# Kernel optimization log

Measured on AMD Instinct MI355X. Metric: run time of the kernel, lower is better.

## Reference

```python
import jax, jax.numpy as jnp
import numpy as np
from math import pi, sqrt, factorial

NUM_SPHERICAL = 7
NUM_RADIAL = 6
CUTOFF = 5.0


def _sph_jn_np(x, n):
    # spherical Bessel j_n(x) in float64 numpy via upward recurrence
    x = np.asarray(x, dtype=np.float64)
    jm = np.sin(x) / x
    if n == 0:
        return jm
    jc = np.sin(x) / x**2 - np.cos(x) / x
    for l in range(2, n + 1):
        jm, jc = jc, (2 * l - 1) / x * jc - jm
    return jc


def _jn_zeros(n, k):
    # first k positive zeros of j_l for l = 0..n-1 (zeros of j_l interleave those of j_{l-1})
    nz = k + n
    z = np.zeros((n, nz))
    z[0] = np.arange(1, nz + 1) * np.pi
    for l in range(1, n):
        for j in range(nz - l):
            a, b = z[l - 1, j], z[l - 1, j + 1]
            fa = _sph_jn_np(a, l)
            for _ in range(100):
                m = 0.5 * (a + b)
                fm = _sph_jn_np(m, l)
                if fa * fm <= 0:
                    b = m
                else:
                    a, fa = m, fm
            z[l, j] = 0.5 * (a + b)
    return z[:, :k]


_ZEROS_NP = _jn_zeros(NUM_SPHERICAL, NUM_RADIAL)  # (n, k)
_NORM_NP = np.array([[(0.5 * _sph_jn_np(_ZEROS_NP[l, j], l + 1) ** 2) ** -0.5
                      for j in range(NUM_RADIAL)] for l in range(NUM_SPHERICAL)])
BESSEL_ZEROS = jnp.asarray(_ZEROS_NP, dtype=jnp.float32)  # z_{l,j}
BESSEL_NORM = jnp.asarray(_NORM_NP, dtype=jnp.float32)    # sqrt(2)/|j_{l+1}(z_{l,j})|


def _rbf(dist):
    # normalized spherical Bessel basis: rbf[:, l*k + j] = norm[l,j] * j_l(z_{l,j} * dist/cutoff)
    d = dist / CUTOFF
    u = d[:, None, None] * BESSEL_ZEROS[None]  # (E, n, k)
    cols = []
    for l in range(NUM_SPHERICAL):
        x = u[:, l, :]
        jm = jnp.sin(x) / x  # j_0
        if l == 0:
            jc = jm
        else:
            jc = jnp.sin(x) / (x * x) - jnp.cos(x) / x  # j_1
        for ll in range(2, l + 1):
            jm, jc = jc, (2 * ll - 1) / x * jc - jm
        cols.append(BESSEL_NORM[l] * jc)
    return jnp.concatenate(cols, axis=1)  # (E, n*k)


def _cbf(angle, phi):
    # real spherical harmonics Y_{l,m}(angle, phi), flat order m = -l..l per l
    n = NUM_SPHERICAL
    z = jnp.cos(angle)
    s = jnp.sin(angle)
    P = {(0, 0): jnp.ones_like(z)}
    for m in range(1, n):
        P[(m, m)] = (1 - 2 * m) * s * P[(m - 1, m - 1)]  # Condon-Shortley phase included
    for m in range(0, n - 1):
        P[(m + 1, m)] = (2 * m + 1) * z * P[(m, m)]
    for m in range(n):
        for l in range(m + 2, n):
            P[(l, m)] = ((2 * l - 1) * z * P[(l - 1, m)] - (l + m - 1) * P[(l - 2, m)]) / (l - m)

    def pref(l, m):
        return sqrt((2 * l + 1) * factorial(l - m) / (4.0 * pi * factorial(l + m)))

    cols = [jnp.full_like(angle, 0.5 / sqrt(pi))]  # Y_00 constant
    for l in range(1, n):
        for m in range(-l, l + 1):
            am = abs(m)
            if m < 0:
                cols.append(sqrt(2.0) * pref(l, am) * jnp.sin(am * phi) * P[(l, am)])
            elif m == 0:
                cols.append(pref(l, 0) * P[(l, 0)])
            else:
                cols.append(sqrt(2.0) * pref(l, am) * jnp.cos(am * phi) * P[(l, am)])
    return jnp.stack(cols, axis=1)  # (T, n*n)


def setup_inputs() -> dict:
    key = jax.random.key(0)
    kd, ka, kp, ki = jax.random.split(key, 4)
    E, T = 150000, 500000
    dist = jax.random.uniform(kd, (E,), minval=0.5, maxval=5.0, dtype=jnp.float32)
    angle = jax.random.uniform(ka, (T,), minval=0.0, maxval=float(np.pi), dtype=jnp.float32)
    phi = jax.random.uniform(kp, (T,), minval=-float(np.pi), maxval=float(np.pi), dtype=jnp.float32)
    idx_kj = jax.random.randint(ki, (T,), 0, E)
    return {"dist": dist, "angle": angle, "phi": phi, "idx_kj": idx_kj}


def reference(dist, angle, phi, idx_kj):
    n, k = NUM_SPHERICAL, NUM_RADIAL
    rbf = _rbf(dist)          # (E, n*k)
    cbf = _cbf(angle, phi)    # (T, n*n)
    out = (rbf[idx_kj].reshape(-1, 1, n, k) * cbf.reshape(-1, n, n, 1)).reshape(-1, n * n * k)
    return out
```

## Files before the change

### kernel.cpp

```cpp
#include <hip/hip_runtime.h>
#include <math.h>

#ifndef M_PI
#define M_PI 3.14159265358979323846
#endif

#define NS 7
#define NK 6
#define GT 64
#define BT 256
#define NC (NS*NS)
#define NR (NS*NK)
#define NF2 147

typedef float f32x2 __attribute__((ext_vector_type(2)));
typedef float f32x4 __attribute__((ext_vector_type(4)));


__device__ void jl_pair_f(float x, int l, float& jl, float& jm1) {
  float s, c;
  __sincosf(x, &s, &c);
  float invx = 1.0f / x;
  float j0 = s * invx, jm = c * invx;
  if (l == 0) { jl = j0; jm1 = jm; return; }
  float j1 = (s * invx - c) * invx;
  for (int ll = 2; ll <= l; ++ll) {
    float t = (2.0f * ll - 1.0f) * invx * j1 - j0;
    j0 = j1; j1 = t;
  }
  jl = j1; jm1 = j0;
}

__global__ void setup_kernel(float* tab) {
  int id = threadIdx.x;
  if (id < NS * NK) {
    int l = id / NK, j = id % NK;
    float nu = l + 0.5f, mu = 4.0f * nu * nu;
    float b  = ((float)(j + 1) + 0.5f * nu - 0.25f) * (float)M_PI;
    float b8 = 8.0f * b;
    float x = b - (mu - 1.0f) / b8
                - 4.0f * (mu - 1.0f) * (7.0f * mu - 31.0f) / (3.0f * b8 * b8 * b8)
                - 32.0f * (mu - 1.0f) * (83.0f * mu * mu - 982.0f * mu + 3779.0f) /
                  (15.0f * b8 * b8 * b8 * b8 * b8);
    float jl, jm1;
    for (int it = 0; it < 5; ++it) {
      jl_pair_f(x, l, jl, jm1);
      float dj = jm1 - (l + 1.0f) / x * jl;
      x -= jl / dj;
    }
    tab[id] = x;
    jl_pair_f(x, l, jl, jm1);
    float jp1 = (2.0f * l + 1.0f) / x * jl - jm1;
    tab[NS * NK + id] = sqrtf(2.0f) / fabsf(jp1);
  }
  if (id < NC) {
    double v;
    if (id == 0) {
      v = 0.5 / sqrt(M_PI);
    } else {
      int l = 1;
      while ((l + 1) * (l + 1) <= id) ++l;
      int m  = id - l * l - l;
      int am = m < 0 ? -m : m;
      double fr = 1.0;
      for (int i2 = l - am + 1; i2 <= l + am; ++i2) fr *= (double)i2;
      double pref = sqrt((2.0 * l + 1.0) / (4.0 * M_PI * fr));
      v = (m != 0) ? sqrt(2.0) * pref : pref;
    }
    tab[2 * NS * NK + id] = (float)v;
  }
}

__global__ __launch_bounds__(BT, 6) void torsion_kernel(
    const float* __restrict__ dist, const float* __restrict__ angle,
    const float* __restrict__ phi, const int* __restrict__ idx_kj,
    const float* __restrict__ tab, float* __restrict__ out, int T) {
  __shared__ float s_cbf[GT][NC];
  __shared__ __align__(8) float s_rbf[GT][NR];
  __shared__ float s_d[GT];
  __shared__ float s_tab[133];
  __shared__ unsigned s_map2[NF2];

  const int tid = threadIdx.x;
  const int t0  = blockIdx.x * GT;
  const int nt  = min(GT, T - t0);

  float a = 0.0f, ph = 0.0f;
  if (tid < GT) {
    int t = t0 + tid;
    float dd = 1.0f;
    if (t < T) {
      dd = dist[idx_kj[t]] * 0.2f;
      a  = angle[t];
      ph = phi[t];
    }
    s_d[tid] = dd;
  }
  if (tid < 133) s_tab[tid] = tab[tid];
  if (tid < NF2) {
    auto mk = [](int cc) {
      int ii = (cc * 3121) >> 16;
      int rem2 = cc - 21 * ii;
      int jj = (rem2 * 86) >> 8;
      return (unsigned)((ii * NS + jj) | (rem2 << 8));
    };
    int cc1 = tid + 1; if (cc1 == NF2) cc1 = 0;
    s_map2[tid] = mk(tid) | (mk(cc1) << 16);
  }
  __syncthreads();

  if (tid < GT) {
    if (t0 + tid < T) {
      float z, s;
      __sincosf(a, &s, &z);
      float sp, cp;
      __sincosf(ph, &sp, &cp);
      float cmv[NS], smv[NS];
      cmv[0] = 1.0f; smv[0] = 0.0f;
      cmv[1] = cp;   smv[1] = sp;
#pragma unroll
      for (int m = 2; m < NS; ++m) {
        cmv[m] = 2.0f * cp * cmv[m - 1] - cmv[m - 2];
        smv[m] = 2.0f * cp * smv[m - 1] - smv[m - 2];
      }
      const float* coef = s_tab + 2 * NR;
      float* crow = s_cbf[tid];
      float pmm = 1.0f;
#pragma unroll
      for (int m = 0; m < NS; ++m) {
        float pl1 = pmm, pl2 = 0.0f;
#pragma unroll
        for (int l = m; l < NS; ++l) {
          float plm;
          if (l == m)          plm = pmm;
          else if (l == m + 1) plm = (float)(2 * m + 1) * z * pmm;
          else                 plm = ((float)(2 * l - 1) * z * pl1 -
                                      (float)(l + m - 1) * pl2) *
                                     (float)(1.0 / (double)(l - m));
          int cpn = l * l + l + m;
          if (m == 0) {
            crow[cpn] = coef[cpn] * plm;
          } else {
            crow[cpn] = coef[cpn] * cmv[m] * plm;
            crow[l * l + l - m] = coef[l * l + l - m] * smv[m] * plm;
          }
          pl2 = pl1; pl1 = plm;
        }
        pmm = (float)(-1 - 2 * m) * s * pmm;
      }
    }
  } else {
    int j  = tid - 64;
    int t  = j / NR;
    int cc = j - NR * t;
    int i2 = j;
    float* rlin = &s_rbf[0][0];
#pragma unroll 2
    for (int it = 0; it < 14; ++it) {
      int l = (cc * 43) >> 8;
      float x = s_d[t] * s_tab[cc];
      float sx, cx;
      __sincosf(x, &sx, &cx);
      float invx = 1.0f / x;
      float jm = sx * invx;
      float jc;
      if (l == 0) jc = jm;
      else {
        jc = (sx * invx - cx) * invx;
#pragma unroll
        for (int ll = 2; ll <= 6; ++ll) {
          if (ll <= l) {
            float tt = (float)(2 * ll - 1) * invx * jc - jm;
            jm = jc; jc = tt;
          }
        }
      }
      rlin[i2] = s_tab[NR + cc] * jc;
      i2 += 192;
      cc += 24; t += 4;
      if (cc >= NR) { cc -= NR; ++t; }
    }
  }
  __syncthreads();

  const f32x2* r2 = (const f32x2*)&s_rbf[0][0];

  if (nt == GT) {
    const int w    = tid >> 6;
    const int lane = tid & 63;
    const int n0   = w * 1176 + lane;
    int p = n0 / 147;
    int k = n0 - 147 * p;
    int cc = k << 1; if (cc >= NF2) cc -= NF2;

    f32x4* o4 = (f32x4*)out + (size_t)blockIdx.x * 4704 + n0;

    auto GATHER = [&]() -> f32x4 {
      int t2 = p << 1;
      int ta = t2 + (k >= 74 ? 1 : 0);
      int tb = t2 + (k >= 73 ? 1 : 0);
      unsigned mp = s_map2[cc];
      unsigned i0 = mp & 0xffu,          r0 = (mp >> 8) & 0xffu;
      unsigned i1 = (mp >> 16) & 0xffu,  r1 = mp >> 24;
      float cv0 = s_cbf[ta][i0];
      f32x2 rv0 = r2[ta * 21 + r0];
      float cv1 = s_cbf[tb][i1];
      f32x2 rv1 = r2[tb * 21 + r1];
      f32x4 ov = {cv0 * rv0.x, cv0 * rv0.y, cv1 * rv1.x, cv1 * rv1.y};
      k += 64;  if (k >= 147) { k -= 147; ++p; }
      cc += 128; if (cc >= NF2) cc -= NF2;
      return ov;
    };

    f32x4 ov[6];
#pragma unroll
    for (int g = 0; g < 3; ++g) {
#pragma unroll
      for (int j = 0; j < 6; ++j) ov[j] = GATHER();
#pragma unroll
      for (int j = 0; j < 6; ++j)
        __builtin_nontemporal_store(ov[j], o4 + (g * 6 + j) * 64);
    }
    if (lane < 24) {
      f32x4 last = GATHER();
      __builtin_nontemporal_store(last, o4 + 18 * 64);
    }
  } else {
    f32x2* o2 = (f32x2*)out + (size_t)t0 * NF2;
    int tot = nt * NF2;
    for (int i = tid; i < tot; i += BT) {
      int t  = i / NF2;
      int c2 = i - NF2 * t;
      unsigned mp = s_map2[c2] & 0xffffu;
      float cv = s_cbf[t][mp & 0xffu];
      f32x2 rv = r2[t * 21 + (mp >> 8)];
      f32x2 ov = cv * rv;
      __builtin_nontemporal_store(ov, o2 + i);
    }
  }
}

extern "C" void kernel_launch(void* const* d_in, const int* in_sizes, int n_in,
                              void* d_out, int out_size, void* d_ws, size_t ws_size,
                              hipStream_t stream) {
  const float* dist  = (const float*)d_in[0];
  const float* angle = (const float*)d_in[1];
  const float* phi   = (const float*)d_in[2];
  const int*   idx   = (const int*)d_in[3];
  float* out = (float*)d_out;
  float* tab = (float*)d_ws;
  int T = in_sizes[1];

  hipLaunchKernelGGL(setup_kernel, dim3(1), dim3(64), 0, stream, tab);
  int nb = (T + GT - 1) / GT;
  hipLaunchKernelGGL(torsion_kernel, dim3(nb), dim3(BT), 0, stream,
                     dist, angle, phi, idx, tab, out, T);
}
```

Baseline: 122.8 us.

## Make each wavefront process its own 16 triplets, removing the block-wide barrier

```diff
diff --git a/kernel.cpp b/kernel.cpp
--- a/kernel.cpp
+++ b/kernel.cpp
@@ -75,27 +75,17 @@
     const float* __restrict__ dist, const float* __restrict__ angle,
     const float* __restrict__ phi, const int* __restrict__ idx_kj,
     const float* __restrict__ tab, float* __restrict__ out, int T) {
-  __shared__ float s_cbf[GT][NC];
-  __shared__ __align__(8) float s_rbf[GT][NR];
-  __shared__ float s_d[GT];
+  __shared__ float s_cbf[4][16][NC];
+  __shared__ __align__(8) float s_rbf[4][16][NR];
+  __shared__ float s_dw[4][16];
   __shared__ float s_tab[133];
   __shared__ unsigned s_map2[NF2];
 
-  const int tid = threadIdx.x;
-  const int t0  = blockIdx.x * GT;
-  const int nt  = min(GT, T - t0);
-
-  float a = 0.0f, ph = 0.0f;
-  if (tid < GT) {
-    int t = t0 + tid;
-    float dd = 1.0f;
-    if (t < T) {
-      dd = dist[idx_kj[t]] * 0.2f;
-      a  = angle[t];
-      ph = phi[t];
-    }
-    s_d[tid] = dd;
-  }
+  const int tid  = threadIdx.x;
+  const int w    = tid >> 6;
+  const int lane = tid & 63;
+  const int tw   = blockIdx.x * GT + w * 16;
+
   if (tid < 133) s_tab[tid] = tab[tid];
   if (tid < NF2) {
     auto mk = [](int cc) {
@@ -109,8 +99,21 @@
   }
   __syncthreads();
 
-  if (tid < GT) {
-    if (t0 + tid < T) {
+  float a = 0.0f, ph = 0.0f;
+  if (lane < 16) {
+    int t = tw + lane;
+    float dd = 1.0f;
+    if (t < T) {
+      dd = dist[idx_kj[t]] * 0.2f;
+      a  = angle[t];
+      ph = phi[t];
+    }
+    s_dw[w][lane] = dd;
+  }
+  asm volatile("s_waitcnt lgkmcnt(0)" ::: "memory");
+
+  if (lane < 16) {
+    if (tw + lane < T) {
       float z, s;
       __sincosf(a, &s, &z);
       float sp, cp;
@@ -124,7 +127,7 @@
         smv[m] = 2.0f * cp * smv[m - 1] - smv[m - 2];
       }
       const float* coef = s_tab + 2 * NR;
-      float* crow = s_cbf[tid];
+      float* crow = s_cbf[w][lane];
       float pmm = 1.0f;
 #pragma unroll
       for (int m = 0; m < NS; ++m) {
@@ -150,15 +153,15 @@
       }
     }
   } else {
-    int j  = tid - 64;
+    int j  = lane - 16;
     int t  = j / NR;
     int cc = j - NR * t;
     int i2 = j;
-    float* rlin = &s_rbf[0][0];
+    float* rlin = &s_rbf[w][0][0];
 #pragma unroll 2
     for (int it = 0; it < 14; ++it) {
       int l = (cc * 43) >> 8;
-      float x = s_d[t] * s_tab[cc];
+      float x = s_dw[w][t] * s_tab[cc];
       float sx, cx;
       __sincosf(x, &sx, &cx);
       float invx = 1.0f / x;
@@ -176,24 +179,21 @@
         }
       }
       rlin[i2] = s_tab[NR + cc] * jc;
-      i2 += 192;
-      cc += 24; t += 4;
+      i2 += 48;
+      cc += 6; t += 1;
       if (cc >= NR) { cc -= NR; ++t; }
     }
   }
-  __syncthreads();
-
-  const f32x2* r2 = (const f32x2*)&s_rbf[0][0];
-
-  if (nt == GT) {
-    const int w    = tid >> 6;
-    const int lane = tid & 63;
-    const int n0   = w * 1176 + lane;
-    int p = n0 / 147;
-    int k = n0 - 147 * p;
-    int cc = k << 1; if (cc >= NF2) cc -= NF2;
-
-    f32x4* o4 = (f32x4*)out + (size_t)blockIdx.x * 4704 + n0;
+  asm volatile("s_waitcnt lgkmcnt(0)" ::: "memory");
+  __builtin_amdgcn_sched_barrier(0);
+
+  const f32x2* r2 = (const f32x2*)&s_rbf[w][0][0];
+  const int nt_w = min(16, T - tw);
+
+  if (nt_w == 16) {
+    int p = 0, k = lane;
+    int cc = k << 1;
+    f32x4* o4 = (f32x4*)out + (size_t)blockIdx.x * 4704 + w * 1176 + lane;
 
     auto GATHER = [&]() -> f32x4 {
       int t2 = p << 1;
@@ -202,9 +202,9 @@
       unsigned mp = s_map2[cc];
       unsigned i0 = mp & 0xffu,          r0 = (mp >> 8) & 0xffu;
       unsigned i1 = (mp >> 16) & 0xffu,  r1 = mp >> 24;
-      float cv0 = s_cbf[ta][i0];
+      float cv0 = s_cbf[w][ta][i0];
       f32x2 rv0 = r2[ta * 21 + r0];
-      float cv1 = s_cbf[tb][i1];
+      float cv1 = s_cbf[w][tb][i1];
       f32x2 rv1 = r2[tb * 21 + r1];
       f32x4 ov = {cv0 * rv0.x, cv0 * rv0.y, cv1 * rv1.x, cv1 * rv1.y};
       k += 64;  if (k >= 147) { k -= 147; ++p; }
@@ -225,14 +225,14 @@
       f32x4 last = GATHER();
       __builtin_nontemporal_store(last, o4 + 18 * 64);
     }
-  } else {
-    f32x2* o2 = (f32x2*)out + (size_t)t0 * NF2;
-    int tot = nt * NF2;
-    for (int i = tid; i < tot; i += BT) {
+  } else if (nt_w > 0) {
+    f32x2* o2 = (f32x2*)out + (size_t)tw * NF2;
+    int tot = nt_w * NF2;
+    for (int i = lane; i < tot; i += 64) {
       int t  = i / NF2;
       int c2 = i - NF2 * t;
       unsigned mp = s_map2[c2] & 0xffffu;
-      float cv = s_cbf[t][mp & 0xffu];
+      float cv = s_cbf[w][t][mp & 0xffu];
       f32x2 rv = r2[t * 21 + (mp >> 8)];
       f32x2 ov = cv * rv;
       __builtin_nontemporal_store(ov, o2 + i);
```

New measurement: 122.9 us. No clear change (+0.1%).
